# Optimization experiments

Hardware: AMD Instinct MI355X
Metric: run time of the kernel (lower is better)

The kernel has to match this reference:

```python
import jax, jax.numpy as jnp
import numpy as np

N_CONN = 21  # n_connections


def setup_inputs() -> dict:
    key = jax.random.key(0)
    landmarks = jax.random.normal(key, (262144, N_CONN, 3), dtype=jnp.float32)
    return {"landmarks": landmarks}


def reference(landmarks) -> jnp.ndarray:
    # Faithful to the TF layer: connections = [(i, j) for i in range(n) for j in range(n)],
    # connection_vectors[k] = landmarks[:, j_k] - landmarks[:, i_k]; the loop only reads
    # indices k < n, which correspond to pairs (0, k), so v_k = p_k - p_0 (v_0 == 0).
    b, n = landmarks.shape[0], N_CONN
    v = landmarks[:, :n, :] - landmarks[:, :1, :]          # (b, n, d)
    dots = jnp.einsum("bid,bjd->bij", v, v)                 # (b, n, n)
    norms = jnp.linalg.norm(v, axis=-1)                     # (b, n)
    cos = dots / (norms[:, :, None] * norms[:, None, :])    # 0/0 -> nan for v_0
    ang = jnp.arccos(cos)                                   # (b, n, n)
    ang = jnp.where(jnp.isnan(ang), jnp.zeros_like(ang), ang)
    # TF concatenates n*n tensors of shape (batch,) along axis -1 (== axis 0),
    # yielding shape (n*n*batch,) ordered angle-major.
    return ang.reshape(b, n * n).T.reshape(-1)
```

## Files before the change

kernel.cpp:

```cpp
#include <hip/hip_runtime.h>

#define NCONN 21
#define TPB 512
#define BPB 256

typedef float f4 __attribute__((ext_vector_type(4)));

__global__ __launch_bounds__(TPB, 4) void pv_kernel(const float* __restrict__ in,
                                                    float* __restrict__ out,
                                                    int B) {
    __shared__ float lds[BPB * 64];
    const int tid = threadIdx.x;

    const int nwg = gridDim.x;
    int bid = blockIdx.x;
    if ((nwg & 7) == 0) {
        const int cpx = nwg >> 3;
        bid = (bid & 7) * cpx + (bid >> 3);
    }
    const long long blockBatch = (long long)bid * BPB;

    const long long gBase4 = blockBatch * 63 / 4;
    const long long totalF4 = ((long long)B * 63) >> 2;
    const float4* in4 = (const float4*)in;
    #pragma unroll
    for (int it = 0; it < 8; ++it) {
        int t4 = tid + it * TPB;
        if (t4 < (BPB * 63) / 4) {
            long long g4 = gBase4 + t4;
            if (g4 < totalF4) {
                float4 v = in4[g4];
                float vals[4] = {v.x, v.y, v.z, v.w};
                int f = 4 * t4;
                #pragma unroll
                for (int q = 0; q < 4; ++q) {
                    int f2 = f + q;
                    int r  = f2 / 63;
                    int c  = f2 - r * 63;
                    lds[r * 64 + ((c + (r >> 2)) & 63)] = vals[q];
                }
            }
        }
    }
    __syncthreads();

    if (tid < BPB && blockBatch + tid < B) {
        float* row = lds + tid * 64;
        const int rot = tid >> 2;
        const float p0x = row[(0 + rot) & 63];
        const float p0y = row[(1 + rot) & 63];
        const float p0z = row[(2 + rot) & 63];
        #pragma unroll
        for (int e = 1; e < NCONN; ++e) {
            const int s0 = (3 * e + 0 + rot) & 63;
            const int s1 = (3 * e + 1 + rot) & 63;
            const int s2 = (3 * e + 2 + rot) & 63;
            float vx = row[s0] - p0x;
            float vy = row[s1] - p0y;
            float vz = row[s2] - p0z;
            float d  = fmaf(vx, vx, fmaf(vy, vy, vz * vz));
            float rr = rsqrtf(d);
            row[s0] = vx * rr;
            row[s1] = vy * rr;
            row[s2] = vz * rr;
        }
    }
    __syncthreads();

    const int l = tid & 63;
    const int w = tid >> 6;
    const int rowb = 4 * l;
    const long long remLL = B - blockBatch;
    const int rem = (int)(remLL < BPB ? remLL : (long long)BPB);
    const bool fullv = (rowb + 4 <= rem);
    float* op = out + blockBatch + rowb;
    const size_t sB = (size_t)B;

    {
        const f4 z4 = {0.f, 0.f, 0.f, 0.f};
        for (int idx = w; idx < 41; idx += 8) {
            const int p = (idx < 21) ? idx : (idx - 20) * NCONN;
            float* dst = op + (size_t)p * sB;
            if (fullv) {
                __builtin_nontemporal_store(z4, (f4*)dst);
            } else {
                for (int k = 0; rowb + k < rem; ++k) dst[k] = 0.0f;
            }
        }
    }

    for (int idx = w; idx < 400; idx += 8) {
        const int i = idx / 20 + 1;
        const int j = idx - (i - 1) * 20 + 1;
        f4 ang;
        #pragma unroll
        for (int k = 0; k < 4; ++k) {
            const float* row = lds + (rowb + k) * 64;
            const float uix = row[(3 * i + 0 + l) & 63];
            const float uiy = row[(3 * i + 1 + l) & 63];
            const float uiz = row[(3 * i + 2 + l) & 63];
            const float ujx = row[(3 * j + 0 + l) & 63];
            const float ujy = row[(3 * j + 1 + l) & 63];
            const float ujz = row[(3 * j + 2 + l) & 63];
            float c = fmaf(uix, ujx, fmaf(uiy, ujy, uiz * ujz));
            c = fmaxf(fminf(c, 1.0f), -1.0f);
            float t = fabsf(c);
            float s = sqrtf(1.0f - t);
            float p = fmaf(t, -0.0187293f, 0.0742610f);
            p = fmaf(t, p, -0.2121144f);
            p = fmaf(t, p, 1.5707288f);
            float rr = s * p;
            ang[k] = (c >= 0.0f) ? rr : (3.14159265358979f - rr);
        }
        float* dst = op + (size_t)(i * NCONN + j) * sB;
        if (fullv) {
            __builtin_nontemporal_store(ang, (f4*)dst);
        } else {
            for (int k = 0; rowb + k < rem; ++k) dst[k] = ang[k];
        }
    }
}

extern "C" void kernel_launch(void* const* d_in, const int* in_sizes, int n_in,
                              void* d_out, int out_size, void* d_ws, size_t ws_size,
                              hipStream_t stream) {
    const float* in = (const float*)d_in[0];
    float* out = (float*)d_out;
    const int B = in_sizes[0] / (NCONN * 3);
    const int grid = (B + BPB - 1) / BPB;
    hipLaunchKernelGGL(pv_kernel, dim3(grid), dim3(TPB), 0, stream, in, out, B);
}
```

Baseline: 508.2 us.

## Split into plane-transpose kernel and row-wise angle kernel via workspace

Replaces the single fused kernel with two kernels. The first normalizes the vectors and writes them to a workspace as structure-of-arrays planes (60 x B). The second has each wave own two output rows i across a span of the batch, reusing the i-vectors in registers while streaming j-planes from global memory, so each wave writes long contiguous runs of output rows. The goal is better write locality and less LDS work, at the cost of extra workspace traffic (writing and re-reading 60*B floats) and a second launch. The old fused kernel remains as a fallback when the workspace is too small or B is not a multiple of 4096.

```diff
diff --git a/kernel.cpp b/kernel.cpp
--- a/kernel.cpp
+++ b/kernel.cpp
@@ -1,32 +1,141 @@
 #include <hip/hip_runtime.h>
 
 #define NCONN 21
-#define TPB 512
-#define BPB 256
 
 typedef float f4 __attribute__((ext_vector_type(4)));
 
-__global__ __launch_bounds__(TPB, 4) void pv_kernel(const float* __restrict__ in,
-                                                    float* __restrict__ out,
-                                                    int B) {
-    __shared__ float lds[BPB * 64];
+__device__ __forceinline__ float acos_poly(float c) {
+    c = fmaxf(fminf(c, 1.0f), -1.0f);
+    float t = fabsf(c);
+    float s = sqrtf(1.0f - t);
+    float p = fmaf(t, -0.0187293f, 0.0742610f);
+    p = fmaf(t, p, -0.2121144f);
+    p = fmaf(t, p, 1.5707288f);
+    float r = s * p;
+    return (c >= 0.0f) ? r : (3.14159265358979f - r);
+}
+
+__global__ __launch_bounds__(256, 2) void k1_planes(const float* __restrict__ in,
+                                                    float* __restrict__ ws, int B) {
+    __shared__ float lds[256 * 64];
     const int tid = threadIdx.x;
-
-    const int nwg = gridDim.x;
-    int bid = blockIdx.x;
-    if ((nwg & 7) == 0) {
-        const int cpx = nwg >> 3;
-        bid = (bid & 7) * cpx + (bid >> 3);
-    }
-    const long long blockBatch = (long long)bid * BPB;
+    const long long blockBatch = (long long)blockIdx.x * 256;
+
+    const long long gBase4 = blockBatch * 63 / 4;
+    const float4* in4 = (const float4*)in;
+    #pragma unroll
+    for (int it = 0; it < 16; ++it) {
+        int t4 = tid + it * 256;
+        if (t4 < 4032) {
+            float4 v = in4[gBase4 + t4];
+            float vals[4] = {v.x, v.y, v.z, v.w};
+            int f = 4 * t4;
+            #pragma unroll
+            for (int q = 0; q < 4; ++q) {
+                int f2 = f + q;
+                int r  = f2 / 63;
+                int c  = f2 - r * 63;
+                lds[r * 64 + ((c + (r >> 2)) & 63)] = vals[q];
+            }
+        }
+    }
+    __syncthreads();
+
+    {
+        float* row = lds + tid * 64;
+        const int rot = tid >> 2;
+        const float p0x = row[(0 + rot) & 63];
+        const float p0y = row[(1 + rot) & 63];
+        const float p0z = row[(2 + rot) & 63];
+        #pragma unroll
+        for (int e = 1; e < NCONN; ++e) {
+            const int s0 = (3 * e + 0 + rot) & 63;
+            const int s1 = (3 * e + 1 + rot) & 63;
+            const int s2 = (3 * e + 2 + rot) & 63;
+            float vx = row[s0] - p0x;
+            float vy = row[s1] - p0y;
+            float vz = row[s2] - p0z;
+            float d  = fmaf(vx, vx, fmaf(vy, vy, vz * vz));
+            float rr = rsqrtf(d);
+            row[s0] = vx * rr;
+            row[s1] = vy * rr;
+            row[s2] = vz * rr;
+        }
+    }
+    __syncthreads();
+
+    const int l = tid & 63, w = tid >> 6;
+    const int rowb = 4 * l;
+    for (int q = w; q < 60; q += 4) {
+        f4 val;
+        #pragma unroll
+        for (int k = 0; k < 4; ++k)
+            val[k] = lds[(rowb + k) * 64 + ((q + 3 + l) & 63)];
+        *(f4*)(ws + (size_t)q * B + blockBatch + rowb) = val;
+    }
+}
+
+#define SPAN 1024
+__global__ __launch_bounds__(256) void k2_rows(const float* __restrict__ ws,
+                                               float* __restrict__ out, int B) {
+    const int tid = threadIdx.x;
+    const int l = tid & 63;
+    const int W = blockIdx.x * 4 + (tid >> 6);
+    const int unit = W % 11;
+    const int sp = W / 11;
+    const long long b0 = (long long)sp * SPAN;
+    const size_t sB = (size_t)B;
+    const f4 z4 = {0.f, 0.f, 0.f, 0.f};
+
+    for (int ch = 0; ch < SPAN / 256; ++ch) {
+        const long long lb = b0 + ch * 256 + 4 * l;
+        if (unit == 10) {
+            for (int j = 0; j < NCONN; ++j)
+                __builtin_nontemporal_store(z4, (f4*)(out + (size_t)j * sB + lb));
+        } else {
+            const int i0 = 2 * unit + 1, i1 = i0 + 1;
+            const float* pw = ws + lb;
+            const f4 ax = *(const f4*)(pw + (size_t)(3 * (i0 - 1) + 0) * sB);
+            const f4 ay = *(const f4*)(pw + (size_t)(3 * (i0 - 1) + 1) * sB);
+            const f4 az = *(const f4*)(pw + (size_t)(3 * (i0 - 1) + 2) * sB);
+            const f4 bx = *(const f4*)(pw + (size_t)(3 * (i1 - 1) + 0) * sB);
+            const f4 by = *(const f4*)(pw + (size_t)(3 * (i1 - 1) + 1) * sB);
+            const f4 bz = *(const f4*)(pw + (size_t)(3 * (i1 - 1) + 2) * sB);
+            __builtin_nontemporal_store(z4, (f4*)(out + (size_t)(i0 * NCONN) * sB + lb));
+            __builtin_nontemporal_store(z4, (f4*)(out + (size_t)(i1 * NCONN) * sB + lb));
+            for (int j = 1; j < NCONN; ++j) {
+                const f4 jx = *(const f4*)(pw + (size_t)(3 * (j - 1) + 0) * sB);
+                const f4 jy = *(const f4*)(pw + (size_t)(3 * (j - 1) + 1) * sB);
+                const f4 jz = *(const f4*)(pw + (size_t)(3 * (j - 1) + 2) * sB);
+                f4 a0, a1;
+                #pragma unroll
+                for (int k = 0; k < 4; ++k) {
+                    a0[k] = acos_poly(fmaf(ax[k], jx[k], fmaf(ay[k], jy[k], az[k] * jz[k])));
+                    a1[k] = acos_poly(fmaf(bx[k], jx[k], fmaf(by[k], jy[k], bz[k] * jz[k])));
+                }
+                __builtin_nontemporal_store(a0, (f4*)(out + (size_t)(i0 * NCONN + j) * sB + lb));
+                __builtin_nontemporal_store(a1, (f4*)(out + (size_t)(i1 * NCONN + j) * sB + lb));
+            }
+        }
+    }
+}
+
+#define FTPB 512
+#define FBPB 256
+__global__ __launch_bounds__(FTPB, 4) void pv_fallback(const float* __restrict__ in,
+                                                       float* __restrict__ out,
+                                                       int B) {
+    __shared__ float lds[FBPB * 64];
+    const int tid = threadIdx.x;
+    const long long blockBatch = (long long)blockIdx.x * FBPB;
 
     const long long gBase4 = blockBatch * 63 / 4;
     const long long totalF4 = ((long long)B * 63) >> 2;
     const float4* in4 = (const float4*)in;
     #pragma unroll
     for (int it = 0; it < 8; ++it) {
-        int t4 = tid + it * TPB;
-        if (t4 < (BPB * 63) / 4) {
+        int t4 = tid + it * FTPB;
+        if (t4 < (FBPB * 63) / 4) {
             long long g4 = gBase4 + t4;
             if (g4 < totalF4) {
                 float4 v = in4[g4];
@@ -44,7 +153,7 @@
     }
     __syncthreads();
 
-    if (tid < BPB && blockBatch + tid < B) {
+    if (tid < FBPB && blockBatch + tid < B) {
         float* row = lds + tid * 64;
         const int rot = tid >> 2;
         const float p0x = row[(0 + rot) & 63];
@@ -71,7 +180,7 @@
     const int w = tid >> 6;
     const int rowb = 4 * l;
     const long long remLL = B - blockBatch;
-    const int rem = (int)(remLL < BPB ? remLL : (long long)BPB);
+    const int rem = (int)(remLL < FBPB ? remLL : (long long)FBPB);
     const bool fullv = (rowb + 4 <= rem);
     float* op = out + blockBatch + rowb;
     const size_t sB = (size_t)B;
@@ -81,11 +190,8 @@
         for (int idx = w; idx < 41; idx += 8) {
             const int p = (idx < 21) ? idx : (idx - 20) * NCONN;
             float* dst = op + (size_t)p * sB;
-            if (fullv) {
-                __builtin_nontemporal_store(z4, (f4*)dst);
-            } else {
-                for (int k = 0; rowb + k < rem; ++k) dst[k] = 0.0f;
-            }
+            if (fullv) __builtin_nontemporal_store(z4, (f4*)dst);
+            else for (int k = 0; rowb + k < rem; ++k) dst[k] = 0.0f;
         }
     }
 
@@ -102,22 +208,11 @@
             const float ujx = row[(3 * j + 0 + l) & 63];
             const float ujy = row[(3 * j + 1 + l) & 63];
             const float ujz = row[(3 * j + 2 + l) & 63];
-            float c = fmaf(uix, ujx, fmaf(uiy, ujy, uiz * ujz));
-            c = fmaxf(fminf(c, 1.0f), -1.0f);
-            float t = fabsf(c);
-            float s = sqrtf(1.0f - t);
-            float p = fmaf(t, -0.0187293f, 0.0742610f);
-            p = fmaf(t, p, -0.2121144f);
-            p = fmaf(t, p, 1.5707288f);
-            float rr = s * p;
-            ang[k] = (c >= 0.0f) ? rr : (3.14159265358979f - rr);
+            ang[k] = acos_poly(fmaf(uix, ujx, fmaf(uiy, ujy, uiz * ujz)));
         }
         float* dst = op + (size_t)(i * NCONN + j) * sB;
-        if (fullv) {
-            __builtin_nontemporal_store(ang, (f4*)dst);
-        } else {
-            for (int k = 0; rowb + k < rem; ++k) dst[k] = ang[k];
-        }
+        if (fullv) __builtin_nontemporal_store(ang, (f4*)dst);
+        else for (int k = 0; rowb + k < rem; ++k) dst[k] = ang[k];
     }
 }
 
@@ -127,6 +222,15 @@
     const float* in = (const float*)d_in[0];
     float* out = (float*)d_out;
     const int B = in_sizes[0] / (NCONN * 3);
-    const int grid = (B + BPB - 1) / BPB;
-    hipLaunchKernelGGL(pv_kernel, dim3(grid), dim3(TPB), 0, stream, in, out, B);
-}
+    const size_t needWS = (size_t)60 * (size_t)B * sizeof(float);
+
+    if (ws_size >= needWS && (B % 4096) == 0) {
+        float* ws = (float*)d_ws;
+        hipLaunchKernelGGL(k1_planes, dim3(B / 256), dim3(256), 0, stream, in, ws, B);
+        const int waves = 11 * (B / SPAN);
+        hipLaunchKernelGGL(k2_rows, dim3(waves / 4), dim3(256), 0, stream, ws, out, B);
+    } else {
+        const int grid = (B + FBPB - 1) / FBPB;
+        hipLaunchKernelGGL(pv_fallback, dim3(grid), dim3(FTPB), 0, stream, in, out, B);
+    }
+}
```

Result: slower. 544.0 us (+7.0%).
